# Kernel optimization log

Measured on AMD Instinct MI355X. Metric: run time of the kernel, lower is better.

Reference implementation:

```python
import jax, jax.numpy as jnp
import numpy as np

MAX_EMBED = 1024
MAX_HEADS = 16
MIN_WIDTH_RATIO = 0.25


def setup_inputs() -> dict:
    key = jax.random.key(0)
    ks = jax.random.split(key, 10)
    B, S, E = 4, 1024, MAX_EMBED
    query = jax.random.normal(ks[0], (B, S, E), dtype=jnp.float32)
    attention_mask = jax.random.randint(ks[1], (B, 1, 1, S), 0, 2, dtype=jnp.int32)
    # SlimmableLinear params (max sizes); kaiming-ish scale ~ 1/sqrt(fan_in)
    scale = 1.0 / np.sqrt(E)
    def lin(kw, kb):
        w = jax.random.uniform(kw, (E, E), dtype=jnp.float32, minval=-scale, maxval=scale)
        b = jax.random.uniform(kb, (E,), dtype=jnp.float32, minval=-scale, maxval=scale)
        return w, b
    q_w, q_b = lin(ks[2], ks[3])
    k_w, k_b = lin(ks[4], ks[5])
    v_w, v_b = lin(ks[6], ks[7])
    o_w, o_b = lin(ks[8], ks[9])
    return {"query": query, "attention_mask": attention_mask,
            "q_w": q_w, "q_b": q_b, "k_w": k_w, "k_b": k_b,
            "v_w": v_w, "v_b": v_b, "o_w": o_w, "o_b": o_b,
            "width": 768}


def _slim_linear(x, w, b, width):
    # weight stored [out, in] like torch; slice to [width, width]
    return x[..., :width] @ w[:width, :width].T + b[:width]


def reference(query, attention_mask, q_w, q_b, k_w, k_b, v_w, v_b, o_w, o_b, width):
    min_width = int(MAX_EMBED * MIN_WIDTH_RATIO)
    width = max(min_width, min(int(width), MAX_EMBED))
    num_heads = max(1, width * MAX_HEADS // MAX_EMBED)
    head_dim = width // num_heads
    B, S, _ = query.shape

    q = _slim_linear(query, q_w, q_b, width)  # [B,S,width]
    k = _slim_linear(query, k_w, k_b, width)  # key=query (self-attn)
    v = _slim_linear(query, v_w, v_b, width)

    q = q.reshape(B, S, num_heads, head_dim).transpose(0, 2, 1, 3)  # [B,H,S,D]
    k = k.reshape(B, S, num_heads, head_dim).transpose(0, 2, 1, 3)
    v = v.reshape(B, S, num_heads, head_dim).transpose(0, 2, 1, 3)

    scores = jnp.einsum('bhqd,bhkd->bhqk', q, k) / jnp.sqrt(jnp.float32(head_dim))
    scores = jnp.where(attention_mask == 0, jnp.float32(-1e9), scores)
    attn_weights = jax.nn.softmax(scores, axis=-1)  # [B,H,S,S]
    attn_output = jnp.einsum('bhqk,bhkd->bhqd', attn_weights, v)
    attn_output = attn_output.transpose(0, 2, 1, 3).reshape(B, S, width)
    output = attn_output @ o_w[:width, :width].T + o_b[:width]
    return output, attn_weights
```

## Files before the change

### kernel.cpp

```cpp
#include <hip/hip_runtime.h>

#define Bn 4
#define Sn 1024
#define En 1024
#define Wn 768
#define Hn 12
#define Dn 64

typedef __attribute__((ext_vector_type(8))) short short8;
typedef __attribute__((ext_vector_type(4))) short short4v;
typedef __attribute__((ext_vector_type(4))) float floatx4;

#define MFMA16(A, B, C) __builtin_amdgcn_mfma_f32_16x16x32_bf16(A, B, C, 0, 0, 0)

__device__ __forceinline__ unsigned short f2bf_rn(float f) {
    unsigned int u = __float_as_uint(f);
    unsigned int r = u + 0x7fffu + ((u >> 16) & 1u);
    return (unsigned short)(r >> 16);
}
__device__ __forceinline__ float bf2f(unsigned short h) {
    return __uint_as_float(((unsigned int)h) << 16);
}

__device__ __forceinline__ void gload_lds16(const unsigned short* g, unsigned short* l) {
    __builtin_amdgcn_global_load_lds(
        (const __attribute__((address_space(1))) void*)g,
        (__attribute__((address_space(3))) void*)l, 16, 0, 0);
}

__global__ __launch_bounds__(256) void split_x_kernel(
    const float* __restrict__ x, unsigned short* __restrict__ xh,
    unsigned short* __restrict__ xl)
{
    int e = (blockIdx.x * 256 + threadIdx.x) * 4;
    int row = e / Wn, col = e - row * Wn;
    float4 v = *(const float4*)(x + (size_t)row * En + col);
    float f[4] = {v.x, v.y, v.z, v.w};
    short4v h, l;
    #pragma unroll
    for (int i = 0; i < 4; ++i) {
        unsigned short hh = f2bf_rn(f[i]);
        h[i] = (short)hh;
        l[i] = (short)f2bf_rn(f[i] - bf2f(hh));
    }
    *(short4v*)(xh + e) = h;
    *(short4v*)(xl + e) = l;
}

__global__ __launch_bounds__(256) void split_w_kernel(
    const float* __restrict__ w, unsigned short* __restrict__ dh,
    unsigned short* __restrict__ dl)
{
    int e = (blockIdx.x * 256 + threadIdx.x) * 4;
    int row = e / Wn, col = e - row * Wn;
    float4 v = *(const float4*)(w + (size_t)row * En + col);
    float f[4] = {v.x, v.y, v.z, v.w};
    short4v h, l;
    #pragma unroll
    for (int i = 0; i < 4; ++i) {
        unsigned short hh = f2bf_rn(f[i]);
        h[i] = (short)hh;
        l[i] = (short)f2bf_rn(f[i] - bf2f(hh));
    }
    *(short4v*)(dh + e) = h;
    *(short4v*)(dl + e) = l;
}

__global__ __launch_bounds__(256) void concat_bias_kernel(
    const float* __restrict__ qb, const float* __restrict__ kb,
    const float* __restrict__ vb, float* __restrict__ bq)
{
    int t = blockIdx.x * 256 + threadIdx.x;
    if (t < Wn) bq[t] = qb[t];
    else if (t < 2 * Wn) bq[t] = kb[t - Wn];
    else if (t < 3 * Wn) bq[t] = vb[t - 2 * Wn];
}

__global__ __launch_bounds__(256) void qkv_mfma_kernel(
    const unsigned short* __restrict__ xh, const unsigned short* __restrict__ xl,
    const unsigned short* __restrict__ wh, const unsigned short* __restrict__ wl,
    const float* __restrict__ bq,
    unsigned short* __restrict__ qh_o, unsigned short* __restrict__ ql_o,
    unsigned short* __restrict__ kh_o, unsigned short* __restrict__ kl_o,
    unsigned short* __restrict__ vt_o)
{
    __shared__ __align__(16) unsigned short Ah[128 * 32];
    __shared__ __align__(16) unsigned short Al[128 * 32];
    __shared__ __align__(16) unsigned short Bh[128 * 32];
    __shared__ __align__(16) unsigned short Bl[128 * 32];

    const int tid = threadIdx.x;
    const int wave = tid >> 6, lane = tid & 63;
    const int quad = lane >> 4, l16 = lane & 15;
    const int m0 = blockIdx.x * 128, n0 = blockIdx.y * 128;
    const int wm = wave >> 1, wn = wave & 1;

    floatx4 acc[4][4] = {};

    const unsigned short* gsrc = (wave == 0) ? xh : (wave == 1) ? xl
                               : (wave == 2) ? wh : wl;
    unsigned short* ldst = (wave == 0) ? Ah : (wave == 1) ? Al
                         : (wave == 2) ? Bh : Bl;
    const int base_row = (wave < 2) ? m0 : n0;
    const int r_in = lane >> 2;
    const int cs = (lane & 3) ^ (r_in & 3);

    for (int k0 = 0; k0 < Wn; k0 += 32) {
        #pragma unroll
        for (int i = 0; i < 8; ++i) {
            int r = i * 16 + r_in;
            const unsigned short* gp =
                gsrc + (size_t)(base_row + r) * Wn + k0 + cs * 8;
            gload_lds16(gp, ldst + i * 512);
        }
        __syncthreads();

        short8 afh[4], afl[4], bfh[4], bfl[4];
        #pragma unroll
        for (int t = 0; t < 4; ++t) {
            int mr = wm * 64 + t * 16 + l16;
            int ca = quad ^ (mr & 3);
            afh[t] = *(const short8*)(Ah + mr * 32 + ca * 8);
            afl[t] = *(const short8*)(Al + mr * 32 + ca * 8);
            int nr = wn * 64 + t * 16 + l16;
            int cb = quad ^ (nr & 3);
            bfh[t] = *(const short8*)(Bh + nr * 32 + cb * 8);
            bfl[t] = *(const short8*)(Bl + nr * 32 + cb * 8);
        }
        #pragma unroll
        for (int mt = 0; mt < 4; ++mt)
            #pragma unroll
            for (int nt = 0; nt < 4; ++nt) {
                acc[mt][nt] = MFMA16(afh[mt], bfh[nt], acc[mt][nt]);
                acc[mt][nt] = MFMA16(afh[mt], bfl[nt], acc[mt][nt]);
                acc[mt][nt] = MFMA16(afl[mt], bfh[nt], acc[mt][nt]);
            }
        __syncthreads();
    }

    const int which = n0 / Wn;
    const int b = m0 >> 10;
    #pragma unroll
    for (int nt = 0; nt < 4; ++nt) {
        const int ng = n0 + wn * 64 + nt * 16 + l16;
        const float bias = bq[ng];
        const int f = ng - which * Wn;
        const int h = f >> 6, d = f & 63;
        #pragma unroll
        for (int mt = 0; mt < 4; ++mt) {
            const int mbase = m0 + wm * 64 + mt * 16 + quad * 4;
            const int s0 = mbase & (Sn - 1);
            if (which < 2) {
                unsigned short* oh = which ? kh_o : qh_o;
                unsigned short* ol = which ? kl_o : ql_o;
                size_t idx = (((size_t)(b * Hn + h)) * Sn + s0) * Dn + d;
                #pragma unroll
                for (int r = 0; r < 4; ++r) {
                    float vv = acc[mt][nt][r] + bias;
                    unsigned short hh = f2bf_rn(vv);
                    oh[idx + (size_t)r * Dn] = hh;
                    ol[idx + (size_t)r * Dn] = f2bf_rn(vv - bf2f(hh));
                }
            } else {
                size_t idx = (((size_t)(b * Hn + h)) * Dn + d) * Sn + s0;
                short4v pk;
                #pragma unroll
                for (int r = 0; r < 4; ++r)
                    pk[r] = (short)f2bf_rn(acc[mt][nt][r] + bias);
                *(short4v*)(vt_o + idx) = pk;
            }
        }
    }
}

__global__ __launch_bounds__(256) void attn_mfma_kernel(
    const unsigned short* __restrict__ qh, const unsigned short* __restrict__ ql,
    const unsigned short* __restrict__ kh, const unsigned short* __restrict__ kl,
    const unsigned short* __restrict__ vt, const int* __restrict__ mask,
    float* __restrict__ attn, unsigned short* __restrict__ aoh,
    unsigned short* __restrict__ aol)
{
    __shared__ __align__(16) unsigned short Kh[64 * 72];
    __shared__ __align__(16) unsigned short Kl[64 * 72];
    __shared__ __align__(16) unsigned short Vs[64 * 72];
    __shared__ __align__(16) unsigned short Ps[4][16 * 72];
    __shared__ float msk[64];

    const int tid = threadIdx.x;
    const int wave = tid >> 6, lane = tid & 63;
    const int quad = lane >> 4, l16 = lane & 15;
    const int qt = blockIdx.x, h = blockIdx.y, b = blockIdx.z;
    const int bh = b * Hn + h;
    const size_t kvbase = (size_t)bh * Sn * Dn;

    short8 qfh[2], qfl[2];
    {
        const int s = qt * 64 + wave * 16 + l16;
        const size_t off = kvbase + (size_t)s * Dn + quad * 8;
        qfh[0] = *(const short8*)(qh + off);
        qfh[1] = *(const short8*)(qh + off + 32);
        qfl[0] = *(const short8*)(ql + off);
        qfl[1] = *(const short8*)(ql + off + 32);
    }

    const int sr = tid >> 2;
    const int sc = tid & 3;

    float lsum[4] = {0.f, 0.f, 0.f, 0.f};

    for (int kt = 0; kt < 16; ++kt) {
        __syncthreads();
        {
            const size_t g = kvbase + (size_t)(kt * 64 + sr) * Dn + sc * 16;
            *(short8*)&Kh[sr * 72 + sc * 16]     = *(const short8*)(kh + g);
            *(short8*)&Kh[sr * 72 + sc * 16 + 8] = *(const short8*)(kh + g + 8);
            *(short8*)&Kl[sr * 72 + sc * 16]     = *(const short8*)(kl + g);
            *(short8*)&Kl[sr * 72 + sc * 16 + 8] = *(const short8*)(kl + g + 8);
            if (tid < 64) msk[tid] = (float)mask[b * Sn + kt * 64 + tid];
        }
        __syncthreads();
        #pragma unroll
        for (int ct = 0; ct < 4; ++ct) {
            floatx4 acc = {0.f, 0.f, 0.f, 0.f};
            const int key = ct * 16 + l16;
            #pragma unroll
            for (int ks = 0; ks < 2; ++ks) {
                short8 b8h = *(const short8*)&Kh[key * 72 + ks * 32 + quad * 8];
                short8 b8l = *(const short8*)&Kl[key * 72 + ks * 32 + quad * 8];
                acc = MFMA16(qfh[ks], b8h, acc);
                acc = MFMA16(qfh[ks], b8l, acc);
                acc = MFMA16(qfl[ks], b8h, acc);
            }
            const float mv = msk[key];
            #pragma unroll
            for (int r = 0; r < 4; ++r)
                lsum[r] += __expf(acc[r] * 0.125f) * mv;
        }
    }

    #pragma unroll
    for (int r = 0; r < 4; ++r) {
        float v = lsum[r];
        v += __shfl_xor(v, 1, 64);
        v += __shfl_xor(v, 2, 64);
        v += __shfl_xor(v, 4, 64);
        v += __shfl_xor(v, 8, 64);
        lsum[r] = (v > 0.f) ? 1.f / v : 0.f;
    }

    floatx4 oacc[4] = {};
    const size_t vbase = (size_t)bh * Dn * Sn;

    for (int kt = 0; kt < 16; ++kt) {
        __syncthreads();
        {
            const size_t g = kvbase + (size_t)(kt * 64 + sr) * Dn + sc * 16;
            *(short8*)&Kh[sr * 72 + sc * 16]     = *(const short8*)(kh + g);
            *(short8*)&Kh[sr * 72 + sc * 16 + 8] = *(const short8*)(kh + g + 8);
            *(short8*)&Kl[sr * 72 + sc * 16]     = *(const short8*)(kl + g);
            *(short8*)&Kl[sr * 72 + sc * 16 + 8] = *(const short8*)(kl + g + 8);
            const size_t g2 = vbase + (size_t)sr * Sn + kt * 64 + sc * 16;
            *(short8*)&Vs[sr * 72 + sc * 16]     = *(const short8*)(vt + g2);
            *(short8*)&Vs[sr * 72 + sc * 16 + 8] = *(const short8*)(vt + g2 + 8);
            if (tid < 64) msk[tid] = (float)mask[b * Sn + kt * 64 + tid];
        }
        __syncthreads();

        #pragma unroll
        for (int ct = 0; ct < 4; ++ct) {
            floatx4 acc = {0.f, 0.f, 0.f, 0.f};
            const int key = ct * 16 + l16;
            #pragma unroll
            for (int ks = 0; ks < 2; ++ks) {
                short8 b8h = *(const short8*)&Kh[key * 72 + ks * 32 + quad * 8];
                short8 b8l = *(const short8*)&Kl[key * 72 + ks * 32 + quad * 8];
                acc = MFMA16(qfh[ks], b8h, acc);
                acc = MFMA16(qfh[ks], b8l, acc);
                acc = MFMA16(qfl[ks], b8h, acc);
            }
            const float mv = msk[key];
            const int row0 = qt * 64 + wave * 16 + quad * 4;
            const int key_g = kt * 64 + key;
            #pragma unroll
            for (int r = 0; r < 4; ++r) {
                float p = __expf(acc[r] * 0.125f) * mv * lsum[r];
                attn[((size_t)bh * Sn + row0 + r) * Sn + key_g] = p;
                Ps[wave][(quad * 4 + r) * 72 + key] = f2bf_rn(p);
            }
        }
        #pragma unroll
        for (int ks = 0; ks < 2; ++ks) {
            short8 pf = *(const short8*)&Ps[wave][l16 * 72 + ks * 32 + quad * 8];
            #pragma unroll
            for (int dt = 0; dt < 4; ++dt) {
                short8 vf = *(const short8*)&Vs[(dt * 16 + l16) * 72 + ks * 32 + quad * 8];
                oacc[dt] = MFMA16(pf, vf, oacc[dt]);
            }
        }
    }

    const int s0 = qt * 64 + wave * 16 + quad * 4;
    #pragma unroll
    for (int dt = 0; dt < 4; ++dt)
        #pragma unroll
        for (int r = 0; r < 4; ++r) {
            float v = oacc[dt][r];
            size_t idx = ((size_t)(b * Sn + s0 + r)) * Wn + h * Dn + dt * 16 + l16;
            unsigned short hh = f2bf_rn(v);
            aoh[idx] = hh;
            aol[idx] = f2bf_rn(v - bf2f(hh));
        }
}

__global__ __launch_bounds__(256) void oproj_mfma_kernel(
    const unsigned short* __restrict__ aoh, const unsigned short* __restrict__ aol,
    const unsigned short* __restrict__ wh, const unsigned short* __restrict__ wl,
    const float* __restrict__ ob, float* __restrict__ out)
{
    __shared__ __align__(16) unsigned short Ah[128 * 32];
    __shared__ __align__(16) unsigned short Al[128 * 32];
    __shared__ __align__(16) unsigned short Bh[128 * 32];
    __shared__ __align__(16) unsigned short Bl[128 * 32];

    const int tid = threadIdx.x;
    const int wave = tid >> 6, lane = tid & 63;
    const int quad = lane >> 4, l16 = lane & 15;
    const int m0 = blockIdx.x * 128, n0 = blockIdx.y * 128;
    const int wm = wave >> 1, wn = wave & 1;

    floatx4 acc[4][4] = {};

    const unsigned short* gsrc = (wave == 0) ? aoh : (wave == 1) ? aol
                               : (wave == 2) ? wh : wl;
    unsigned short* ldst = (wave == 0) ? Ah : (wave == 1) ? Al
                         : (wave == 2) ? Bh : Bl;
    const int base_row = (wave < 2) ? m0 : n0;
    const int r_in = lane >> 2;
    const int cs = (lane & 3) ^ (r_in & 3);

    for (int k0 = 0; k0 < Wn; k0 += 32) {
        #pragma unroll
        for (int i = 0; i < 8; ++i) {
            int r = i * 16 + r_in;
            const unsigned short* gp =
                gsrc + (size_t)(base_row + r) * Wn + k0 + cs * 8;
            gload_lds16(gp, ldst + i * 512);
        }
        __syncthreads();

        short8 afh[4], afl[4], bfh[4], bfl[4];
        #pragma unroll
        for (int t = 0; t < 4; ++t) {
            int mr = wm * 64 + t * 16 + l16;
            int ca = quad ^ (mr & 3);
            afh[t] = *(const short8*)(Ah + mr * 32 + ca * 8);
            afl[t] = *(const short8*)(Al + mr * 32 + ca * 8);
            int nr = wn * 64 + t * 16 + l16;
            int cb = quad ^ (nr & 3);
            bfh[t] = *(const short8*)(Bh + nr * 32 + cb * 8);
            bfl[t] = *(const short8*)(Bl + nr * 32 + cb * 8);
        }
        #pragma unroll
        for (int mt = 0; mt < 4; ++mt)
            #pragma unroll
            for (int nt = 0; nt < 4; ++nt) {
                acc[mt][nt] = MFMA16(afh[mt], bfh[nt], acc[mt][nt]);
                acc[mt][nt] = MFMA16(afh[mt], bfl[nt], acc[mt][nt]);
                acc[mt][nt] = MFMA16(afl[mt], bfh[nt], acc[mt][nt]);
            }
        __syncthreads();
    }

    #pragma unroll
    for (int nt = 0; nt < 4; ++nt) {
        const int ng = n0 + wn * 64 + nt * 16 + l16;
        const float bias = ob[ng];
        #pragma unroll
        for (int mt = 0; mt < 4; ++mt) {
            const int m = m0 + wm * 64 + mt * 16 + quad * 4;
            #pragma unroll
            for (int r = 0; r < 4; ++r)
                out[(size_t)(m + r) * Wn + ng] = acc[mt][nt][r] + bias;
        }
    }
}

extern "C" void kernel_launch(void* const* d_in, const int* in_sizes, int n_in,
                              void* d_out, int out_size, void* d_ws, size_t ws_size,
                              hipStream_t stream) {
    const float* x    = (const float*)d_in[0];
    const int*   mask = (const int*)  d_in[1];
    const float* qw = (const float*)d_in[2];
    const float* qb = (const float*)d_in[3];
    const float* kw = (const float*)d_in[4];
    const float* kb = (const float*)d_in[5];
    const float* vw = (const float*)d_in[6];
    const float* vb = (const float*)d_in[7];
    const float* ow = (const float*)d_in[8];
    const float* ob = (const float*)d_in[9];

    float* out  = (float*)d_out;
    float* attn = out + (size_t)Bn * Sn * Wn;

    const size_t XE  = (size_t)Bn * Sn * Wn;
    const size_t QKE = (size_t)Bn * Hn * Sn * Dn;
    char* w = (char*)d_ws;
    unsigned short* xh   = (unsigned short*)w;  w += XE * 2;
    unsigned short* xl   = (unsigned short*)w;  w += XE * 2;
    unsigned short* wqh  = (unsigned short*)w;  w += (size_t)3 * Wn * Wn * 2;
    unsigned short* wql  = (unsigned short*)w;  w += (size_t)3 * Wn * Wn * 2;
    unsigned short* woh  = (unsigned short*)w;  w += (size_t)Wn * Wn * 2;
    unsigned short* wol  = (unsigned short*)w;  w += (size_t)Wn * Wn * 2;
    float*          bq   = (float*)w;           w += (size_t)3 * Wn * 4;
    unsigned short* qh_w = (unsigned short*)w;  w += QKE * 2;
    unsigned short* ql_w = (unsigned short*)w;  w += QKE * 2;
    unsigned short* kh_w = (unsigned short*)w;  w += QKE * 2;
    unsigned short* kl_w = (unsigned short*)w;  w += QKE * 2;
    unsigned short* vt_w = (unsigned short*)w;  w += QKE * 2;

    split_x_kernel<<<3072, 256, 0, stream>>>(x, xh, xl);
    split_w_kernel<<<576, 256, 0, stream>>>(qw, wqh, wql);
    split_w_kernel<<<576, 256, 0, stream>>>(kw, wqh + (size_t)Wn * Wn, wql + (size_t)Wn * Wn);
    split_w_kernel<<<576, 256, 0, stream>>>(vw, wqh + (size_t)2 * Wn * Wn, wql + (size_t)2 * Wn * Wn);
    split_w_kernel<<<576, 256, 0, stream>>>(ow, woh, wol);
    concat_bias_kernel<<<9, 256, 0, stream>>>(qb, kb, vb, bq);

    qkv_mfma_kernel<<<dim3(32, 18), 256, 0, stream>>>(
        xh, xl, wqh, wql, bq, qh_w, ql_w, kh_w, kl_w, vt_w);

    attn_mfma_kernel<<<dim3(16, Hn, Bn), 256, 0, stream>>>(
        qh_w, ql_w, kh_w, kl_w, vt_w, mask, attn, xh, xl);

    oproj_mfma_kernel<<<dim3(32, 6), 256, 0, stream>>>(
        xh, xl, woh, wol, ob, out);
}
```

Measured before the change: 451.3 us.

## Halve attention query tile to 32 rows and XOR-swizzle LDS tiles

The attention kernel now uses 128-thread blocks covering 32 query rows, so the grid doubles to 32x12x4 blocks. The K, V and P shared-memory tiles drop their padded 72-element stride in favour of a 64-element stride with an XOR swizzle on 8-element chunks, which keeps bank conflicts low and shrinks LDS use. More blocks should improve occupancy and load balance across CUs. The cost is that each K/V tile is loaded from global memory twice as often, since fewer query rows share each load.

```diff
diff --git a/kernel.cpp b/kernel.cpp
--- a/kernel.cpp
+++ b/kernel.cpp
@@ -173,17 +173,17 @@
     }
 }
 
-__global__ __launch_bounds__(256) void attn_mfma_kernel(
+__global__ __launch_bounds__(128) void attn_mfma_kernel(
     const unsigned short* __restrict__ qh, const unsigned short* __restrict__ ql,
     const unsigned short* __restrict__ kh, const unsigned short* __restrict__ kl,
     const unsigned short* __restrict__ vt, const int* __restrict__ mask,
     float* __restrict__ attn, unsigned short* __restrict__ aoh,
     unsigned short* __restrict__ aol)
 {
-    __shared__ __align__(16) unsigned short Kh[64 * 72];
-    __shared__ __align__(16) unsigned short Kl[64 * 72];
-    __shared__ __align__(16) unsigned short Vs[64 * 72];
-    __shared__ __align__(16) unsigned short Ps[4][16 * 72];
+    __shared__ __align__(16) unsigned short Kh[64 * 64];
+    __shared__ __align__(16) unsigned short Kl[64 * 64];
+    __shared__ __align__(16) unsigned short Vs[64 * 64];
+    __shared__ __align__(16) unsigned short Ps[2][16 * 64];
     __shared__ float msk[64];
 
     const int tid = threadIdx.x;
@@ -195,7 +195,7 @@
 
     short8 qfh[2], qfl[2];
     {
-        const int s = qt * 64 + wave * 16 + l16;
+        const int s = qt * 32 + wave * 16 + l16;
         const size_t off = kvbase + (size_t)s * Dn + quad * 8;
         qfh[0] = *(const short8*)(qh + off);
         qfh[1] = *(const short8*)(qh + off + 32);
@@ -203,19 +203,22 @@
         qfl[1] = *(const short8*)(ql + off + 32);
     }
 
-    const int sr = tid >> 2;
-    const int sc = tid & 3;
+    const int sr = tid >> 1;
+    const int sh = tid & 1;
+    const int swz = sr & 7;
 
     float lsum[4] = {0.f, 0.f, 0.f, 0.f};
 
     for (int kt = 0; kt < 16; ++kt) {
         __syncthreads();
         {
-            const size_t g = kvbase + (size_t)(kt * 64 + sr) * Dn + sc * 16;
-            *(short8*)&Kh[sr * 72 + sc * 16]     = *(const short8*)(kh + g);
-            *(short8*)&Kh[sr * 72 + sc * 16 + 8] = *(const short8*)(kh + g + 8);
-            *(short8*)&Kl[sr * 72 + sc * 16]     = *(const short8*)(kl + g);
-            *(short8*)&Kl[sr * 72 + sc * 16 + 8] = *(const short8*)(kl + g + 8);
+            const size_t g = kvbase + (size_t)(kt * 64 + sr) * Dn + sh * 32;
+            #pragma unroll
+            for (int u = 0; u < 4; ++u) {
+                int pc = (sh * 4 + u) ^ swz;
+                *(short8*)&Kh[sr * 64 + pc * 8] = *(const short8*)(kh + g + u * 8);
+                *(short8*)&Kl[sr * 64 + pc * 8] = *(const short8*)(kl + g + u * 8);
+            }
             if (tid < 64) msk[tid] = (float)mask[b * Sn + kt * 64 + tid];
         }
         __syncthreads();
@@ -225,8 +228,9 @@
             const int key = ct * 16 + l16;
             #pragma unroll
             for (int ks = 0; ks < 2; ++ks) {
-                short8 b8h = *(const short8*)&Kh[key * 72 + ks * 32 + quad * 8];
-                short8 b8l = *(const short8*)&Kl[key * 72 + ks * 32 + quad * 8];
+                const int pc = ((ks * 4 + quad) ^ (l16 & 7)) * 8;
+                short8 b8h = *(const short8*)&Kh[key * 64 + pc];
+                short8 b8l = *(const short8*)&Kl[key * 64 + pc];
                 acc = MFMA16(qfh[ks], b8h, acc);
                 acc = MFMA16(qfh[ks], b8l, acc);
                 acc = MFMA16(qfl[ks], b8h, acc);
@@ -254,14 +258,15 @@
     for (int kt = 0; kt < 16; ++kt) {
         __syncthreads();
         {
-            const size_t g = kvbase + (size_t)(kt * 64 + sr) * Dn + sc * 16;
-            *(short8*)&Kh[sr * 72 + sc * 16]     = *(const short8*)(kh + g);
-            *(short8*)&Kh[sr * 72 + sc * 16 + 8] = *(const short8*)(kh + g + 8);
-            *(short8*)&Kl[sr * 72 + sc * 16]     = *(const short8*)(kl + g);
-            *(short8*)&Kl[sr * 72 + sc * 16 + 8] = *(const short8*)(kl + g + 8);
-            const size_t g2 = vbase + (size_t)sr * Sn + kt * 64 + sc * 16;
-            *(short8*)&Vs[sr * 72 + sc * 16]     = *(const short8*)(vt + g2);
-            *(short8*)&Vs[sr * 72 + sc * 16 + 8] = *(const short8*)(vt + g2 + 8);
+            const size_t g = kvbase + (size_t)(kt * 64 + sr) * Dn + sh * 32;
+            const size_t g2 = vbase + (size_t)sr * Sn + kt * 64 + sh * 32;
+            #pragma unroll
+            for (int u = 0; u < 4; ++u) {
+                int pc = (sh * 4 + u) ^ swz;
+                *(short8*)&Kh[sr * 64 + pc * 8] = *(const short8*)(kh + g + u * 8);
+                *(short8*)&Kl[sr * 64 + pc * 8] = *(const short8*)(kl + g + u * 8);
+                *(short8*)&Vs[sr * 64 + pc * 8] = *(const short8*)(vt + g2 + u * 8);
+            }
             if (tid < 64) msk[tid] = (float)mask[b * Sn + kt * 64 + tid];
         }
         __syncthreads();
@@ -272,34 +277,39 @@
             const int key = ct * 16 + l16;
             #pragma unroll
             for (int ks = 0; ks < 2; ++ks) {
-                short8 b8h = *(const short8*)&Kh[key * 72 + ks * 32 + quad * 8];
-                short8 b8l = *(const short8*)&Kl[key * 72 + ks * 32 + quad * 8];
+                const int pc = ((ks * 4 + quad) ^ (l16 & 7)) * 8;
+                short8 b8h = *(const short8*)&Kh[key * 64 + pc];
+                short8 b8l = *(const short8*)&Kl[key * 64 + pc];
                 acc = MFMA16(qfh[ks], b8h, acc);
                 acc = MFMA16(qfh[ks], b8l, acc);
                 acc = MFMA16(qfl[ks], b8h, acc);
             }
             const float mv = msk[key];
-            const int row0 = qt * 64 + wave * 16 + quad * 4;
+            const int row0 = qt * 32 + wave * 16 + quad * 4;
             const int key_g = kt * 64 + key;
+            const int pchunk = (key >> 3);
             #pragma unroll
             for (int r = 0; r < 4; ++r) {
                 float p = __expf(acc[r] * 0.125f) * mv * lsum[r];
                 attn[((size_t)bh * Sn + row0 + r) * Sn + key_g] = p;
-                Ps[wave][(quad * 4 + r) * 72 + key] = f2bf_rn(p);
+                const int prow = quad * 4 + r;
+                Ps[wave][prow * 64 + ((pchunk ^ (prow & 7)) * 8) + (key & 7)] = f2bf_rn(p);
             }
         }
         #pragma unroll
         for (int ks = 0; ks < 2; ++ks) {
-            short8 pf = *(const short8*)&Ps[wave][l16 * 72 + ks * 32 + quad * 8];
+            const int pc = ((ks * 4 + quad) ^ (l16 & 7)) * 8;
+            short8 pf = *(const short8*)&Ps[wave][l16 * 64 + pc];
             #pragma unroll
             for (int dt = 0; dt < 4; ++dt) {
-                short8 vf = *(const short8*)&Vs[(dt * 16 + l16) * 72 + ks * 32 + quad * 8];
+                const int d = dt * 16 + l16;
+                short8 vf = *(const short8*)&Vs[d * 64 + pc];
                 oacc[dt] = MFMA16(pf, vf, oacc[dt]);
             }
         }
     }
 
-    const int s0 = qt * 64 + wave * 16 + quad * 4;
+    const int s0 = qt * 32 + wave * 16 + quad * 4;
     #pragma unroll
     for (int dt = 0; dt < 4; ++dt)
         #pragma unroll
@@ -428,7 +438,7 @@
     qkv_mfma_kernel<<<dim3(32, 18), 256, 0, stream>>>(
         xh, xl, wqh, wql, bq, qh_w, ql_w, kh_w, kl_w, vt_w);
 
-    attn_mfma_kernel<<<dim3(16, Hn, Bn), 256, 0, stream>>>(
+    attn_mfma_kernel<<<dim3(32, Hn, Bn), 128, 0, stream>>>(
         qh_w, ql_w, kh_w, kl_w, vt_w, mask, attn, xh, xl);
 
     oproj_mfma_kernel<<<dim3(32, 6), 256, 0, stream>>>(
```

Result: slower. 487.7 us (+8.1%).

## Split attention over key chunks, fuse prep kernels, and shrink o-proj tiles

Applied to the files above, without the earlier changes.

Attention is split across four key-range chunks per query tile. Separate kernels compute partial row sums, then the normalized probabilities with partial PV outputs, and a final reduce kernel sums the partial outputs and splits them into bf16 hi/lo. This raises the block count from 768 to 3072 to improve occupancy on the GPU. Q and K are now stored as fp32 and split into hi/lo inside the attention kernels, so QK^T is recomputed in both passes. The five prep launches are merged into one kernel, and the o-proj M tile is halved to 64 rows to double its grid. The cost is extra fp32 traffic for the partial outputs and Q/K, plus two more launches.

```diff
diff --git a/kernel.cpp b/kernel.cpp
--- a/kernel.cpp
+++ b/kernel.cpp
@@ -6,6 +6,7 @@
 #define Wn 768
 #define Hn 12
 #define Dn 64
+#define XE ((size_t)Bn * Sn * Wn)
 
 typedef __attribute__((ext_vector_type(8))) short short8;
 typedef __attribute__((ext_vector_type(4))) short short4v;
@@ -28,13 +29,40 @@
         (__attribute__((address_space(3))) void*)l, 16, 0, 0);
 }
 
-__global__ __launch_bounds__(256) void split_x_kernel(
-    const float* __restrict__ x, unsigned short* __restrict__ xh,
-    unsigned short* __restrict__ xl)
+__global__ __launch_bounds__(256) void prep_kernel(
+    const float* __restrict__ x,
+    const float* __restrict__ qw, const float* __restrict__ kw,
+    const float* __restrict__ vw, const float* __restrict__ ow,
+    const float* __restrict__ qb, const float* __restrict__ kb,
+    const float* __restrict__ vb,
+    unsigned short* __restrict__ xh, unsigned short* __restrict__ xl,
+    unsigned short* __restrict__ wqh, unsigned short* __restrict__ wql,
+    unsigned short* __restrict__ woh, unsigned short* __restrict__ wol,
+    float* __restrict__ bq)
 {
-    int e = (blockIdx.x * 256 + threadIdx.x) * 4;
+    const int bx = blockIdx.x;
+    const float* src; unsigned short *dh, *dl; int e;
+    if (bx < 3072) {
+        e = (bx * 256 + threadIdx.x) * 4;
+        src = x; dh = xh; dl = xl;
+    } else if (bx < 3072 + 1728) {
+        int bb = bx - 3072; int which = bb / 576;
+        e = ((bb - which * 576) * 256 + threadIdx.x) * 4;
+        src = (which == 0) ? qw : (which == 1) ? kw : vw;
+        dh = wqh + (size_t)which * Wn * Wn;
+        dl = wql + (size_t)which * Wn * Wn;
+    } else if (bx < 3072 + 1728 + 576) {
+        e = ((bx - 3072 - 1728) * 256 + threadIdx.x) * 4;
+        src = ow; dh = woh; dl = wol;
+    } else {
+        int t = (bx - 3072 - 1728 - 576) * 256 + threadIdx.x;
+        if (t < Wn) bq[t] = qb[t];
+        else if (t < 2 * Wn) bq[t] = kb[t - Wn];
+        else if (t < 3 * Wn) bq[t] = vb[t - 2 * Wn];
+        return;
+    }
     int row = e / Wn, col = e - row * Wn;
-    float4 v = *(const float4*)(x + (size_t)row * En + col);
+    float4 v = *(const float4*)(src + (size_t)row * En + col);
     float f[4] = {v.x, v.y, v.z, v.w};
     short4v h, l;
     #pragma unroll
@@ -43,45 +71,15 @@
         h[i] = (short)hh;
         l[i] = (short)f2bf_rn(f[i] - bf2f(hh));
     }
-    *(short4v*)(xh + e) = h;
-    *(short4v*)(xl + e) = l;
-}
-
-__global__ __launch_bounds__(256) void split_w_kernel(
-    const float* __restrict__ w, unsigned short* __restrict__ dh,
-    unsigned short* __restrict__ dl)
-{
-    int e = (blockIdx.x * 256 + threadIdx.x) * 4;
-    int row = e / Wn, col = e - row * Wn;
-    float4 v = *(const float4*)(w + (size_t)row * En + col);
-    float f[4] = {v.x, v.y, v.z, v.w};
-    short4v h, l;
-    #pragma unroll
-    for (int i = 0; i < 4; ++i) {
-        unsigned short hh = f2bf_rn(f[i]);
-        h[i] = (short)hh;
-        l[i] = (short)f2bf_rn(f[i] - bf2f(hh));
-    }
     *(short4v*)(dh + e) = h;
     *(short4v*)(dl + e) = l;
-}
-
-__global__ __launch_bounds__(256) void concat_bias_kernel(
-    const float* __restrict__ qb, const float* __restrict__ kb,
-    const float* __restrict__ vb, float* __restrict__ bq)
-{
-    int t = blockIdx.x * 256 + threadIdx.x;
-    if (t < Wn) bq[t] = qb[t];
-    else if (t < 2 * Wn) bq[t] = kb[t - Wn];
-    else if (t < 3 * Wn) bq[t] = vb[t - 2 * Wn];
 }
 
 __global__ __launch_bounds__(256) void qkv_mfma_kernel(
     const unsigned short* __restrict__ xh, const unsigned short* __restrict__ xl,
     const unsigned short* __restrict__ wh, const unsigned short* __restrict__ wl,
     const float* __restrict__ bq,
-    unsigned short* __restrict__ qh_o, unsigned short* __restrict__ ql_o,
-    unsigned short* __restrict__ kh_o, unsigned short* __restrict__ kl_o,
+    float* __restrict__ q32, float* __restrict__ k32,
     unsigned short* __restrict__ vt_o)
 {
     __shared__ __align__(16) unsigned short Ah[128 * 32];
@@ -151,16 +149,11 @@
             const int mbase = m0 + wm * 64 + mt * 16 + quad * 4;
             const int s0 = mbase & (Sn - 1);
             if (which < 2) {
-                unsigned short* oh = which ? kh_o : qh_o;
-                unsigned short* ol = which ? kl_o : ql_o;
+                float* o32 = which ? k32 : q32;
                 size_t idx = (((size_t)(b * Hn + h)) * Sn + s0) * Dn + d;
                 #pragma unroll
-                for (int r = 0; r < 4; ++r) {
-                    float vv = acc[mt][nt][r] + bias;
-                    unsigned short hh = f2bf_rn(vv);
-                    oh[idx + (size_t)r * Dn] = hh;
-                    ol[idx + (size_t)r * Dn] = f2bf_rn(vv - bf2f(hh));
-                }
+                for (int r = 0; r < 4; ++r)
+                    o32[idx + (size_t)r * Dn] = acc[mt][nt][r] + bias;
             } else {
                 size_t idx = (((size_t)(b * Hn + h)) * Dn + d) * Sn + s0;
                 short4v pk;
@@ -173,50 +166,65 @@
     }
 }
 
-__global__ __launch_bounds__(256) void attn_mfma_kernel(
-    const unsigned short* __restrict__ qh, const unsigned short* __restrict__ ql,
-    const unsigned short* __restrict__ kh, const unsigned short* __restrict__ kl,
-    const unsigned short* __restrict__ vt, const int* __restrict__ mask,
-    float* __restrict__ attn, unsigned short* __restrict__ aoh,
-    unsigned short* __restrict__ aol)
+__global__ __launch_bounds__(256) void attn_sum_kernel(
+    const float* __restrict__ q32, const float* __restrict__ k32,
+    const int* __restrict__ mask, float* __restrict__ lpart)
 {
     __shared__ __align__(16) unsigned short Kh[64 * 72];
     __shared__ __align__(16) unsigned short Kl[64 * 72];
-    __shared__ __align__(16) unsigned short Vs[64 * 72];
-    __shared__ __align__(16) unsigned short Ps[4][16 * 72];
     __shared__ float msk[64];
 
     const int tid = threadIdx.x;
     const int wave = tid >> 6, lane = tid & 63;
     const int quad = lane >> 4, l16 = lane & 15;
-    const int qt = blockIdx.x, h = blockIdx.y, b = blockIdx.z;
+    const int qt = blockIdx.x >> 2, ks = blockIdx.x & 3;
+    const int h = blockIdx.y, b = blockIdx.z;
     const int bh = b * Hn + h;
-    const size_t kvbase = (size_t)bh * Sn * Dn;
+    const size_t kvb = (size_t)bh * Sn * Dn;
 
     short8 qfh[2], qfl[2];
     {
         const int s = qt * 64 + wave * 16 + l16;
-        const size_t off = kvbase + (size_t)s * Dn + quad * 8;
-        qfh[0] = *(const short8*)(qh + off);
-        qfh[1] = *(const short8*)(qh + off + 32);
-        qfl[0] = *(const short8*)(ql + off);
-        qfl[1] = *(const short8*)(ql + off + 32);
-    }
-
-    const int sr = tid >> 2;
-    const int sc = tid & 3;
-
+        const float* qp = q32 + kvb + (size_t)s * Dn + quad * 8;
+        #pragma unroll
+        for (int ksp = 0; ksp < 2; ++ksp) {
+            float f[8];
+            *(float4*)&f[0] = *(const float4*)(qp + ksp * 32);
+            *(float4*)&f[4] = *(const float4*)(qp + ksp * 32 + 4);
+            #pragma unroll
+            for (int j = 0; j < 8; ++j) {
+                unsigned short hh = f2bf_rn(f[j]);
+                qfh[ksp][j] = (short)hh;
+                qfl[ksp][j] = (short)f2bf_rn(f[j] - bf2f(hh));
+            }
+        }
+    }
+
+    const int sr = tid >> 2, sc = tid & 3;
     float lsum[4] = {0.f, 0.f, 0.f, 0.f};
 
-    for (int kt = 0; kt < 16; ++kt) {
+    for (int kt = 0; kt < 4; ++kt) {
         __syncthreads();
         {
-            const size_t g = kvbase + (size_t)(kt * 64 + sr) * Dn + sc * 16;
-            *(short8*)&Kh[sr * 72 + sc * 16]     = *(const short8*)(kh + g);
-            *(short8*)&Kh[sr * 72 + sc * 16 + 8] = *(const short8*)(kh + g + 8);
-            *(short8*)&Kl[sr * 72 + sc * 16]     = *(const short8*)(kl + g);
-            *(short8*)&Kl[sr * 72 + sc * 16 + 8] = *(const short8*)(kl + g + 8);
-            if (tid < 64) msk[tid] = (float)mask[b * Sn + kt * 64 + tid];
+            const float* kp = k32 + kvb + (size_t)(ks * 256 + kt * 64 + sr) * Dn + sc * 16;
+            float f[16];
+            *(float4*)&f[0]  = *(const float4*)(kp);
+            *(float4*)&f[4]  = *(const float4*)(kp + 4);
+            *(float4*)&f[8]  = *(const float4*)(kp + 8);
+            *(float4*)&f[12] = *(const float4*)(kp + 12);
+            short8 h0, h1, l0, l1;
+            #pragma unroll
+            for (int j = 0; j < 8; ++j) {
+                unsigned short hh = f2bf_rn(f[j]);
+                h0[j] = (short)hh; l0[j] = (short)f2bf_rn(f[j] - bf2f(hh));
+                unsigned short hh2 = f2bf_rn(f[8 + j]);
+                h1[j] = (short)hh2; l1[j] = (short)f2bf_rn(f[8 + j] - bf2f(hh2));
+            }
+            *(short8*)&Kh[sr * 72 + sc * 16]     = h0;
+            *(short8*)&Kh[sr * 72 + sc * 16 + 8] = h1;
+            *(short8*)&Kl[sr * 72 + sc * 16]     = l0;
+            *(short8*)&Kl[sr * 72 + sc * 16 + 8] = l1;
+            if (tid < 64) msk[tid] = (float)mask[b * Sn + ks * 256 + kt * 64 + tid];
         }
         __syncthreads();
         #pragma unroll
@@ -224,12 +232,12 @@
             floatx4 acc = {0.f, 0.f, 0.f, 0.f};
             const int key = ct * 16 + l16;
             #pragma unroll
-            for (int ks = 0; ks < 2; ++ks) {
-                short8 b8h = *(const short8*)&Kh[key * 72 + ks * 32 + quad * 8];
-                short8 b8l = *(const short8*)&Kl[key * 72 + ks * 32 + quad * 8];
-                acc = MFMA16(qfh[ks], b8h, acc);
-                acc = MFMA16(qfh[ks], b8l, acc);
-                acc = MFMA16(qfl[ks], b8h, acc);
+            for (int ksp = 0; ksp < 2; ++ksp) {
+                short8 b8h = *(const short8*)&Kh[key * 72 + ksp * 32 + quad * 8];
+                short8 b8l = *(const short8*)&Kl[key * 72 + ksp * 32 + quad * 8];
+                acc = MFMA16(qfh[ksp], b8h, acc);
+                acc = MFMA16(qfh[ksp], b8l, acc);
+                acc = MFMA16(qfl[ksp], b8h, acc);
             }
             const float mv = msk[key];
             #pragma unroll
@@ -245,24 +253,96 @@
         v += __shfl_xor(v, 2, 64);
         v += __shfl_xor(v, 4, 64);
         v += __shfl_xor(v, 8, 64);
-        lsum[r] = (v > 0.f) ? 1.f / v : 0.f;
-    }
-
+        lsum[r] = v;
+    }
+    if (l16 == 0) {
+        const int row = qt * 64 + wave * 16 + quad * 4;
+        #pragma unroll
+        for (int r = 0; r < 4; ++r)
+            lpart[((size_t)ks * Bn * Hn + bh) * Sn + row + r] = lsum[r];
+    }
+}
+
+__global__ __launch_bounds__(256) void attn_out_kernel(
+    const float* __restrict__ q32, const float* __restrict__ k32,
+    const unsigned short* __restrict__ vt, const int* __restrict__ mask,
+    const float* __restrict__ lpart, float* __restrict__ attn,
+    float* __restrict__ opart)
+{
+    __shared__ __align__(16) unsigned short Kh[64 * 72];
+    __shared__ __align__(16) unsigned short Kl[64 * 72];
+    __shared__ __align__(16) unsigned short Vs[64 * 72];
+    __shared__ __align__(16) unsigned short Ps[4][16 * 72];
+    __shared__ float msk[64];
+
+    const int tid = threadIdx.x;
+    const int wave = tid >> 6, lane = tid & 63;
+    const int quad = lane >> 4, l16 = lane & 15;
+    const int qt = blockIdx.x >> 2, ks = blockIdx.x & 3;
+    const int h = blockIdx.y, b = blockIdx.z;
+    const int bh = b * Hn + h;
+    const size_t kvb = (size_t)bh * Sn * Dn;
+
+    short8 qfh[2], qfl[2];
+    {
+        const int s = qt * 64 + wave * 16 + l16;
+        const float* qp = q32 + kvb + (size_t)s * Dn + quad * 8;
+        #pragma unroll
+        for (int ksp = 0; ksp < 2; ++ksp) {
+            float f[8];
+            *(float4*)&f[0] = *(const float4*)(qp + ksp * 32);
+            *(float4*)&f[4] = *(const float4*)(qp + ksp * 32 + 4);
+            #pragma unroll
+            for (int j = 0; j < 8; ++j) {
+                unsigned short hh = f2bf_rn(f[j]);
+                qfh[ksp][j] = (short)hh;
+                qfl[ksp][j] = (short)f2bf_rn(f[j] - bf2f(hh));
+            }
+        }
+    }
+
+    float li[4];
+    {
+        const int row = qt * 64 + wave * 16 + quad * 4;
+        #pragma unroll
+        for (int r = 0; r < 4; ++r) {
+            float lv = 0.f;
+            #pragma unroll
+            for (int s4 = 0; s4 < 4; ++s4)
+                lv += lpart[((size_t)s4 * Bn * Hn + bh) * Sn + row + r];
+            li[r] = (lv > 0.f) ? 1.f / lv : 0.f;
+        }
+    }
+
+    const int sr = tid >> 2, sc = tid & 3;
+    const size_t vbase = (size_t)bh * Dn * Sn;
     floatx4 oacc[4] = {};
-    const size_t vbase = (size_t)bh * Dn * Sn;
-
-    for (int kt = 0; kt < 16; ++kt) {
+
+    for (int kt = 0; kt < 4; ++kt) {
         __syncthreads();
         {
-            const size_t g = kvbase + (size_t)(kt * 64 + sr) * Dn + sc * 16;
-            *(short8*)&Kh[sr * 72 + sc * 16]     = *(const short8*)(kh + g);
-            *(short8*)&Kh[sr * 72 + sc * 16 + 8] = *(const short8*)(kh + g + 8);
-            *(short8*)&Kl[sr * 72 + sc * 16]     = *(const short8*)(kl + g);
-            *(short8*)&Kl[sr * 72 + sc * 16 + 8] = *(const short8*)(kl + g + 8);
-            const size_t g2 = vbase + (size_t)sr * Sn + kt * 64 + sc * 16;
+            const float* kp = k32 + kvb + (size_t)(ks * 256 + kt * 64 + sr) * Dn + sc * 16;
+            float f[16];
+            *(float4*)&f[0]  = *(const float4*)(kp);
+            *(float4*)&f[4]  = *(const float4*)(kp + 4);
+            *(float4*)&f[8]  = *(const float4*)(kp + 8);
+            *(float4*)&f[12] = *(const float4*)(kp + 12);
+            short8 h0, h1, l0, l1;
+            #pragma unroll
+            for (int j = 0; j < 8; ++j) {
+                unsigned short hh = f2bf_rn(f[j]);
+                h0[j] = (short)hh; l0[j] = (short)f2bf_rn(f[j] - bf2f(hh));
+                unsigned short hh2 = f2bf_rn(f[8 + j]);
+                h1[j] = (short)hh2; l1[j] = (short)f2bf_rn(f[8 + j] - bf2f(hh2));
+            }
+            *(short8*)&Kh[sr * 72 + sc * 16]     = h0;
+            *(short8*)&Kh[sr * 72 + sc * 16 + 8] = h1;
+            *(short8*)&Kl[sr * 72 + sc * 16]     = l0;
+            *(short8*)&Kl[sr * 72 + sc * 16 + 8] = l1;
+            const size_t g2 = vbase + (size_t)sr * Sn + ks * 256 + kt * 64 + sc * 16;
             *(short8*)&Vs[sr * 72 + sc * 16]     = *(const short8*)(vt + g2);
             *(short8*)&Vs[sr * 72 + sc * 16 + 8] = *(const short8*)(vt + g2 + 8);
-            if (tid < 64) msk[tid] = (float)mask[b * Sn + kt * 64 + tid];
+            if (tid < 64) msk[tid] = (float)mask[b * Sn + ks * 256 + kt * 64 + tid];
         }
         __syncthreads();
 
@@ -271,29 +351,29 @@
             floatx4 acc = {0.f, 0.f, 0.f, 0.f};
             const int key = ct * 16 + l16;
             #pragma unroll
-            for (int ks = 0; ks < 2; ++ks) {
-                short8 b8h = *(const short8*)&Kh[key * 72 + ks * 32 + quad * 8];
-                short8 b8l = *(const short8*)&Kl[key * 72 + ks * 32 + quad * 8];
-                acc = MFMA16(qfh[ks], b8h, acc);
-                acc = MFMA16(qfh[ks], b8l, acc);
-                acc = MFMA16(qfl[ks], b8h, acc);
+            for (int ksp = 0; ksp < 2; ++ksp) {
+                short8 b8h = *(const short8*)&Kh[key * 72 + ksp * 32 + quad * 8];
+                short8 b8l = *(const short8*)&Kl[key * 72 + ksp * 32 + quad * 8];
+                acc = MFMA16(qfh[ksp], b8h, acc);
+                acc = MFMA16(qfh[ksp], b8l, acc);
+                acc = MFMA16(qfl[ksp], b8h, acc);
             }
             const float mv = msk[key];
             const int row0 = qt * 64 + wave * 16 + quad * 4;
-            const int key_g = kt * 64 + key;
+            const int key_g = ks * 256 + kt * 64 + key;
             #pragma unroll
             for (int r = 0; r < 4; ++r) {
-                float p = __expf(acc[r] * 0.125f) * mv * lsum[r];
+                float p = __expf(acc[r] * 0.125f) * mv * li[r];
                 attn[((size_t)bh * Sn + row0 + r) * Sn + key_g] = p;
                 Ps[wave][(quad * 4 + r) * 72 + key] = f2bf_rn(p);
             }
         }
         #pragma unroll
-        for (int ks = 0; ks < 2; ++ks) {
-            short8 pf = *(const short8*)&Ps[wave][l16 * 72 + ks * 32 + quad * 8];
+        for (int ksp = 0; ksp < 2; ++ksp) {
+            short8 pf = *(const short8*)&Ps[wave][l16 * 72 + ksp * 32 + quad * 8];
             #pragma unroll
             for (int dt = 0; dt < 4; ++dt) {
-                short8 vf = *(const short8*)&Vs[(dt * 16 + l16) * 72 + ks * 32 + quad * 8];
+                short8 vf = *(const short8*)&Vs[(dt * 16 + l16) * 72 + ksp * 32 + quad * 8];
                 oacc[dt] = MFMA16(pf, vf, oacc[dt]);
             }
         }
@@ -303,13 +383,31 @@
     #pragma unroll
     for (int dt = 0; dt < 4; ++dt)
         #pragma unroll
-        for (int r = 0; r < 4; ++r) {
-            float v = oacc[dt][r];
-            size_t idx = ((size_t)(b * Sn + s0 + r)) * Wn + h * Dn + dt * 16 + l16;
-            unsigned short hh = f2bf_rn(v);
-            aoh[idx] = hh;
-            aol[idx] = f2bf_rn(v - bf2f(hh));
-        }
+        for (int r = 0; r < 4; ++r)
+            opart[(size_t)ks * XE + ((size_t)b * Sn + s0 + r) * Wn
+                  + h * Dn + dt * 16 + l16] = oacc[dt][r];
+}
+
+__global__ __launch_bounds__(256) void reduce_ao_kernel(
+    const float* __restrict__ opart, unsigned short* __restrict__ aoh,
+    unsigned short* __restrict__ aol)
+{
+    size_t e = ((size_t)blockIdx.x * 256 + threadIdx.x) * 4;
+    float4 a0 = *(const float4*)(opart + e);
+    float4 a1 = *(const float4*)(opart + XE + e);
+    float4 a2 = *(const float4*)(opart + 2 * XE + e);
+    float4 a3 = *(const float4*)(opart + 3 * XE + e);
+    float f[4] = {a0.x + a1.x + a2.x + a3.x, a0.y + a1.y + a2.y + a3.y,
+                  a0.z + a1.z + a2.z + a3.z, a0.w + a1.w + a2.w + a3.w};
+    short4v h, l;
+    #pragma unroll
+    for (int i = 0; i < 4; ++i) {
+        unsigned short hh = f2bf_rn(f[i]);
+        h[i] = (short)hh;
+        l[i] = (short)f2bf_rn(f[i] - bf2f(hh));
+    }
+    *(short4v*)(aoh + e) = h;
+    *(short4v*)(aol + e) = l;
 }
 
 __global__ __launch_bounds__(256) void oproj_mfma_kernel(
@@ -317,51 +415,61 @@
     const unsigned short* __restrict__ wh, const unsigned short* __restrict__ wl,
     const float* __restrict__ ob, float* __restrict__ out)
 {
-    __shared__ __align__(16) unsigned short Ah[128 * 32];
-    __shared__ __align__(16) unsigned short Al[128 * 32];
+    __shared__ __align__(16) unsigned short Ah[64 * 32];
+    __shared__ __align__(16) unsigned short Al[64 * 32];
     __shared__ __align__(16) unsigned short Bh[128 * 32];
     __shared__ __align__(16) unsigned short Bl[128 * 32];
 
     const int tid = threadIdx.x;
     const int wave = tid >> 6, lane = tid & 63;
     const int quad = lane >> 4, l16 = lane & 15;
-    const int m0 = blockIdx.x * 128, n0 = blockIdx.y * 128;
+    const int m0 = blockIdx.x * 64, n0 = blockIdx.y * 128;
     const int wm = wave >> 1, wn = wave & 1;
 
-    floatx4 acc[4][4] = {};
-
-    const unsigned short* gsrc = (wave == 0) ? aoh : (wave == 1) ? aol
-                               : (wave == 2) ? wh : wl;
-    unsigned short* ldst = (wave == 0) ? Ah : (wave == 1) ? Al
-                         : (wave == 2) ? Bh : Bl;
-    const int base_row = (wave < 2) ? m0 : n0;
+    floatx4 acc[2][4] = {};
+
     const int r_in = lane >> 2;
     const int cs = (lane & 3) ^ (r_in & 3);
 
     for (int k0 = 0; k0 < Wn; k0 += 32) {
-        #pragma unroll
-        for (int i = 0; i < 8; ++i) {
-            int r = i * 16 + r_in;
-            const unsigned short* gp =
-                gsrc + (size_t)(base_row + r) * Wn + k0 + cs * 8;
-            gload_lds16(gp, ldst + i * 512);
-        }
-        __syncthreads();
-
-        short8 afh[4], afl[4], bfh[4], bfl[4];
-        #pragma unroll
-        for (int t = 0; t < 4; ++t) {
-            int mr = wm * 64 + t * 16 + l16;
+        if (wave == 0) {
+            #pragma unroll
+            for (int i = 0; i < 4; ++i) {
+                gload_lds16(aoh + (size_t)(m0 + i * 16 + r_in) * Wn + k0 + cs * 8,
+                            Ah + i * 512);
+                gload_lds16(aol + (size_t)(m0 + i * 16 + r_in) * Wn + k0 + cs * 8,
+                            Al + i * 512);
+            }
+        } else if (wave == 1) {
+            #pragma unroll
+            for (int i = 0; i < 8; ++i)
+                gload_lds16(wh + (size_t)(n0 + i * 16 + r_in) * Wn + k0 + cs * 8,
+                            Bh + i * 512);
+        } else if (wave == 2) {
+            #pragma unroll
+            for (int i = 0; i < 8; ++i)
+                gload_lds16(wl + (size_t)(n0 + i * 16 + r_in) * Wn + k0 + cs * 8,
+                            Bl + i * 512);
+        }
+        __syncthreads();
+
+        short8 afh[2], afl[2], bfh[4], bfl[4];
+        #pragma unroll
+        for (int t = 0; t < 2; ++t) {
+            int mr = wm * 32 + t * 16 + l16;
             int ca = quad ^ (mr & 3);
             afh[t] = *(const short8*)(Ah + mr * 32 + ca * 8);
             afl[t] = *(const short8*)(Al + mr * 32 + ca * 8);
+        }
+        #pragma unroll
+        for (int t = 0; t < 4; ++t) {
             int nr = wn * 64 + t * 16 + l16;
             int cb = quad ^ (nr & 3);
             bfh[t] = *(const short8*)(Bh + nr * 32 + cb * 8);
             bfl[t] = *(const short8*)(Bl + nr * 32 + cb * 8);
         }
         #pragma unroll
-        for (int mt = 0; mt < 4; ++mt)
+        for (int mt = 0; mt < 2; ++mt)
             #pragma unroll
             for (int nt = 0; nt < 4; ++nt) {
                 acc[mt][nt] = MFMA16(afh[mt], bfh[nt], acc[mt][nt]);
@@ -376,8 +484,8 @@
         const int ng = n0 + wn * 64 + nt * 16 + l16;
         const float bias = ob[ng];
         #pragma unroll
-        for (int mt = 0; mt < 4; ++mt) {
-            const int m = m0 + wm * 64 + mt * 16 + quad * 4;
+        for (int mt = 0; mt < 2; ++mt) {
+            const int m = m0 + wm * 32 + mt * 16 + quad * 4;
             #pragma unroll
             for (int r = 0; r < 4; ++r)
                 out[(size_t)(m + r) * Wn + ng] = acc[mt][nt][r] + bias;
@@ -400,10 +508,8 @@
     const float* ob = (const float*)d_in[9];
 
     float* out  = (float*)d_out;
-    float* attn = out + (size_t)Bn * Sn * Wn;
-
-    const size_t XE  = (size_t)Bn * Sn * Wn;
-    const size_t QKE = (size_t)Bn * Hn * Sn * Dn;
+    float* attn = out + XE;
+
     char* w = (char*)d_ws;
     unsigned short* xh   = (unsigned short*)w;  w += XE * 2;
     unsigned short* xl   = (unsigned short*)w;  w += XE * 2;
@@ -412,25 +518,26 @@
     unsigned short* woh  = (unsigned short*)w;  w += (size_t)Wn * Wn * 2;
     unsigned short* wol  = (unsigned short*)w;  w += (size_t)Wn * Wn * 2;
     float*          bq   = (float*)w;           w += (size_t)3 * Wn * 4;
-    unsigned short* qh_w = (unsigned short*)w;  w += QKE * 2;
-    unsigned short* ql_w = (unsigned short*)w;  w += QKE * 2;
-    unsigned short* kh_w = (unsigned short*)w;  w += QKE * 2;
-    unsigned short* kl_w = (unsigned short*)w;  w += QKE * 2;
-    unsigned short* vt_w = (unsigned short*)w;  w += QKE * 2;
-
-    split_x_kernel<<<3072, 256, 0, stream>>>(x, xh, xl);
-    split_w_kernel<<<576, 256, 0, stream>>>(qw, wqh, wql);
-    split_w_kernel<<<576, 256, 0, stream>>>(kw, wqh + (size_t)Wn * Wn, wql + (size_t)Wn * Wn);
-    split_w_kernel<<<576, 256, 0, stream>>>(vw, wqh + (size_t)2 * Wn * Wn, wql + (size_t)2 * Wn * Wn);
-    split_w_kernel<<<576, 256, 0, stream>>>(ow, woh, wol);
-    concat_bias_kernel<<<9, 256, 0, stream>>>(qb, kb, vb, bq);
+    float*          q32  = (float*)w;           w += XE * 4;
+    float*          k32  = (float*)w;           w += XE * 4;
+    unsigned short* vt_w = (unsigned short*)w;  w += XE * 2;
+    float*          lpart = (float*)w;          w += (size_t)4 * Bn * Hn * Sn * 4;
+    float*          opart = (float*)w;          w += (size_t)4 * XE * 4;
+
+    prep_kernel<<<5385, 256, 0, stream>>>(x, qw, kw, vw, ow, qb, kb, vb,
+                                          xh, xl, wqh, wql, woh, wol, bq);
 
     qkv_mfma_kernel<<<dim3(32, 18), 256, 0, stream>>>(
-        xh, xl, wqh, wql, bq, qh_w, ql_w, kh_w, kl_w, vt_w);
-
-    attn_mfma_kernel<<<dim3(16, Hn, Bn), 256, 0, stream>>>(
-        qh_w, ql_w, kh_w, kl_w, vt_w, mask, attn, xh, xl);
-
-    oproj_mfma_kernel<<<dim3(32, 6), 256, 0, stream>>>(
+        xh, xl, wqh, wql, bq, q32, k32, vt_w);
+
+    attn_sum_kernel<<<dim3(64, Hn, Bn), 256, 0, stream>>>(
+        q32, k32, mask, lpart);
+
+    attn_out_kernel<<<dim3(64, Hn, Bn), 256, 0, stream>>>(
+        q32, k32, vt_w, mask, lpart, attn, opart);
+
+    reduce_ao_kernel<<<3072, 256, 0, stream>>>(opart, xh, xl);
+
+    oproj_mfma_kernel<<<dim3(64, 6), 256, 0, stream>>>(
         xh, xl, woh, wol, ob, out);
 }
```

New measurement: 451.2 us. No clear change (-0.0%).
